# Optimization experiments

Measured on AMD Instinct MI355X. Metric: run time of the kernel, lower is better.

Reference implementation:

```python
import jax, jax.numpy as jnp
import numpy as np

B, S, H, NH = 2, 2048, 1024, 16
HD = H // NH  # head dim = 64


def setup_inputs() -> dict:
    key = jax.random.key(0)
    ks = jax.random.split(key, 11)
    s = 1.0 / np.sqrt(H)
    return {
        "q": jax.random.normal(ks[0], (B, S, H), jnp.float32),
        "k": jax.random.normal(ks[1], (B, S, H), jnp.float32),
        "v": jax.random.normal(ks[2], (B, S, H), jnp.float32),
        "Wq": jax.random.normal(ks[3], (H, H), jnp.float32) * s,
        "bq": jax.random.normal(ks[4], (H,), jnp.float32) * 0.02,
        "Wk": jax.random.normal(ks[5], (H, H), jnp.float32) * s,
        "bk": jax.random.normal(ks[6], (H,), jnp.float32) * 0.02,
        "Wv": jax.random.normal(ks[7], (H, H), jnp.float32) * s,
        "bv": jax.random.normal(ks[8], (H,), jnp.float32) * 0.02,
        "Wo": jax.random.normal(ks[9], (H, H), jnp.float32) * s,
        "bo": jax.random.normal(ks[10], (H,), jnp.float32) * 0.02,
    }


def reference(q, k, v, Wq, bq, Wk, bk, Wv, bv, Wo, bo):
    # QKV projections: [B,S,H]
    qp = q @ Wq + bq
    kp = k @ Wk + bk
    vp = v @ Wv + bv
    # split heads -> [B, NH, S, HD]
    def split(x):
        return x.reshape(B, S, NH, HD).transpose(0, 2, 1, 3)
    qh, kh, vh = split(qp), split(kp), split(vp)
    # scores [B, NH, S, S], scale by sqrt(head_dim)
    scores = jnp.einsum('bhqd,bhkd->bhqk', qh, kh) / jnp.sqrt(jnp.asarray(HD, qh.dtype))
    attn = jax.nn.softmax(scores, axis=-1)  # attention_dropout p=0.0 (eval)
    ctx = jnp.einsum('bhqk,bhkd->bhqd', attn, vh)
    # merge heads -> [B, S, H]
    ctx = ctx.transpose(0, 2, 1, 3).reshape(B, S, H)
    out = ctx @ Wo + bo  # dropout p=0.0 (eval)
    return out
```

## Files before the change

kernel.cpp:

```cpp
#include <hip/hip_runtime.h>

typedef unsigned short u16;
typedef __attribute__((ext_vector_type(8))) short bf16x8;
typedef __attribute__((ext_vector_type(4))) float f32x4;
typedef __attribute__((ext_vector_type(16))) float f32x16;
typedef __attribute__((ext_vector_type(4))) unsigned short u16x4;
typedef __attribute__((ext_vector_type(4))) unsigned int u32x4;

#define B_  2
#define S_  2048
#define H_  1024
#define NH_ 16
#define HD_ 64
#define MR_ (B_*S_)
#define K_  H_

__device__ __forceinline__ u16 f2bf(float f) {
  union { float f; unsigned u; } x; x.f = f;
  unsigned r = x.u + 0x7fffu + ((x.u >> 16) & 1u);
  return (u16)(r >> 16);
}

__device__ __forceinline__ unsigned cvtpk(float lo, float hi) {
  unsigned r;
  asm("v_cvt_pk_bf16_f32 %0, %1, %2" : "=v"(r) : "v"(lo), "v"(hi));
  return r;
}

__device__ __forceinline__ void plswap(unsigned &a, unsigned &b) {
  asm("v_permlane32_swap_b32 %0, %1" : "+v"(a), "+v"(b));
}

__device__ __forceinline__ void gload16(const u16* g, u16* l) {
  __builtin_amdgcn_global_load_lds((const __attribute__((address_space(1))) void*)g,
                                   (__attribute__((address_space(3))) void*)l, 16, 0, 0);
}

__global__ __launch_bounds__(256) void prep(const float* __restrict__ q, const float* __restrict__ k,
                                            const float* __restrict__ v, const float* __restrict__ Wq,
                                            const float* __restrict__ Wk, const float* __restrict__ Wv,
                                            const float* __restrict__ Wo, u16* __restrict__ dst,
                                            u16* __restrict__ wt) {
  __shared__ float t[32][33];
  const int bid = blockIdx.x;
  if (bid < 12288) {
    const int z = bid >> 12;
    const float* src = z == 0 ? q : z == 1 ? k : v;
    u16* d = dst + (size_t)z * MR_ * H_;
    size_t i = ((size_t)(bid & 4095) * 256 + threadIdx.x) * 4;
    float4 f = *(const float4*)(src + i);
    u16x4 o = { f2bf(f.x), f2bf(f.y), f2bf(f.z), f2bf(f.w) };
    *(u16x4*)(d + i) = o;
  } else {
    const int r = bid - 12288;
    const int z = r >> 10;
    const float* W = z == 0 ? Wq : z == 1 ? Wk : z == 2 ? Wv : Wo;
    u16* Wt = wt + (size_t)z * H_ * K_;
    const int n0 = (r & 31) * 32, k0 = ((r >> 5) & 31) * 32;
    const int tx = threadIdx.x & 31, ty = threadIdx.x >> 5;
    #pragma unroll
    for (int i = 0; i < 4; i++) t[ty + 8*i][tx] = W[(size_t)(k0 + ty + 8*i) * H_ + n0 + tx];
    __syncthreads();
    #pragma unroll
    for (int i = 0; i < 4; i++) Wt[(size_t)(n0 + ty + 8*i) * K_ + k0 + tx] = f2bf(t[tx][ty + 8*i]);
  }
}

template <int MODE>
__device__ __forceinline__ void gemm_body(const u16* __restrict__ A, const u16* __restrict__ Bt,
                                          const float* __restrict__ bias, float scale,
                                          u16* __restrict__ Obf, float* __restrict__ Of,
                                          int m_tile, int n_tile) {
  __shared__ u16 ldsA[128 * 64];
  __shared__ u16 ldsB[128 * 64];
  const int tid = threadIdx.x;
  const int lane = tid & 63, wave = tid >> 6;
  const int wm = wave >> 1, wn = wave & 1;
  const int m0 = m_tile * 128, n0 = n_tile * 128;

  f32x4 acc[4][4] = {};

  const int srow = tid >> 3;
  const int sslot = (tid & 7) ^ (srow & 7);
  const u16* ga = A + (size_t)(m0 + srow) * K_ + sslot * 8;
  const u16* gb = Bt + (size_t)(n0 + srow) * K_ + sslot * 8;
  u16* la = ldsA + tid * 8;
  u16* lb = ldsB + tid * 8;

  const int fr = lane & 15;
  const int kg = lane >> 4;

  for (int k0 = 0; k0 < K_; k0 += 64) {
    #pragma unroll
    for (int j = 0; j < 4; j++) gload16(ga + (size_t)(j * 32) * K_ + k0, la + j * 2048);
    #pragma unroll
    for (int j = 0; j < 4; j++) gload16(gb + (size_t)(j * 32) * K_ + k0, lb + j * 2048);
    __syncthreads();

    #pragma unroll
    for (int kk = 0; kk < 2; kk++) {
      const int ps = (((kk << 2) | kg) ^ (fr & 7)) * 8;
      bf16x8 a[4], b[4];
      #pragma unroll
      for (int mf = 0; mf < 4; mf++)
        a[mf] = *(const bf16x8*)&ldsA[(wm * 64 + mf * 16 + fr) * 64 + ps];
      #pragma unroll
      for (int nf = 0; nf < 4; nf++)
        b[nf] = *(const bf16x8*)&ldsB[(wn * 64 + nf * 16 + fr) * 64 + ps];
      #pragma unroll
      for (int mf = 0; mf < 4; mf++)
        #pragma unroll
        for (int nf = 0; nf < 4; nf++)
          acc[mf][nf] = __builtin_amdgcn_mfma_f32_16x16x32_bf16(a[mf], b[nf], acc[mf][nf], 0, 0, 0);
    }
    __syncthreads();
  }

  float bcol[4];
  #pragma unroll
  for (int nf = 0; nf < 4; nf++) bcol[nf] = bias[n0 + wn * 64 + nf * 16 + fr];

  if (MODE == 2) {
    #pragma unroll
    for (int mf = 0; mf < 4; mf++) {
      const int row0 = m0 + wm * 64 + mf * 16 + kg * 4;
      #pragma unroll
      for (int nf = 0; nf < 4; nf++) {
        const int col = n0 + wn * 64 + nf * 16 + fr;
        u16x4 o;
        #pragma unroll
        for (int r = 0; r < 4; r++) o[r] = f2bf(acc[mf][nf][r] + bcol[nf]);
        size_t idx = (((size_t)(col + ((row0 >> 11) << 10))) << 11) + (row0 & 2047);
        *(u16x4*)(Obf + idx) = o;
      }
    }
  } else {
    #pragma unroll
    for (int mf = 0; mf < 4; mf++)
      #pragma unroll
      for (int r = 0; r < 4; r++) {
        const int row = m0 + wm * 64 + mf * 16 + kg * 4 + r;
        #pragma unroll
        for (int nf = 0; nf < 4; nf++) {
          const int col = n0 + wn * 64 + nf * 16 + fr;
          float val = (acc[mf][nf][r] + bcol[nf]) * scale;
          if (MODE == 0) Obf[(size_t)row * H_ + col] = f2bf(val);
          else           Of [(size_t)row * H_ + col] = val;
        }
      }
  }
}

__device__ __forceinline__ void gemm_tiles(int &m_tile, int &n_tile) {
  const int bid = blockIdx.x + (blockIdx.y << 3);
  const int swz = ((bid & 7) << 5) + (bid >> 3);
  m_tile = swz >> 3;
  n_tile = swz & 7;
}

__global__ __launch_bounds__(256) void gemm_qkv(const u16* __restrict__ xb, const u16* __restrict__ wt,
                                                const float* __restrict__ b0, const float* __restrict__ b1,
                                                const float* __restrict__ b2,
                                                u16* __restrict__ QKo, u16* __restrict__ VTo) {
  const int z = blockIdx.z;
  const u16* A = xb + (size_t)z * MR_ * K_;
  const u16* Bt = wt + (size_t)z * H_ * K_;
  int mt, nt;
  gemm_tiles(mt, nt);
  if (z == 2) {
    gemm_body<2>(A, Bt, b2, 1.0f, VTo, nullptr, mt, nt);
  } else {
    const float* bias = z == 0 ? b0 : b1;
    const float scale = z == 0 ? 0.18033688011112042f : 1.0f;
    gemm_body<0>(A, Bt, bias, scale, QKo + (size_t)z * MR_ * H_, nullptr, mt, nt);
  }
}

__global__ __launch_bounds__(256) void gemm_out(const u16* __restrict__ ctx, const u16* __restrict__ wot,
                                                const float* __restrict__ bo, float* __restrict__ out) {
  int mt, nt;
  gemm_tiles(mt, nt);
  gemm_body<1>(ctx, wot, bo, 1.0f, nullptr, out, mt, nt);
}

__global__ __launch_bounds__(512, 4) void attn(const u16* __restrict__ qp, const u16* __restrict__ kp,
                                               const u16* __restrict__ vt, u16* __restrict__ ctx) {
  __shared__ u16 Kl[2][2][64 * 64];
  __shared__ u16 Vl[2][2][64 * 64];
  __shared__ float mlbuf[2][4][32][2];
  const int bid = blockIdx.x + (blockIdx.y << 4);
  const int swz = ((bid & 7) << 6) + (bid >> 3);
  const int bh = swz >> 4;
  const int b = bh >> 4, h = bh & 15;
  const int q0 = (swz & 15) * 128;
  const int tid = threadIdx.x;
  const int g0 = tid >> 8;
  const int gt = tid & 255;
  const int w = (tid >> 6) & 3;
  const int l = tid & 63;
  const int ql = l & 31, hi = l >> 5;

  const u16* Q   = qp + (size_t)b * S_ * H_ + h * HD_;
  const u16* Kb  = kp + (size_t)b * S_ * H_ + h * HD_;
  const u16* Vtb = vt + (size_t)bh * HD_ * S_;
  u16* O = ctx + (size_t)b * S_ * H_ + h * HD_;

  const int srow = gt >> 3;
  const int sslot = (gt & 7) ^ (srow & 7);
  const int sbase = g0 << 10;

  const u16* Qrow = Q + (size_t)(q0 + w * 32 + ql) * H_;

  f32x16 oacc0 = {}, oacc1 = {};
  float m_run = -1e30f, l_run = 0.f;

  #pragma unroll
  for (int j = 0; j < 2; j++) {
    gload16(Kb + (size_t)(sbase + srow + 32 * j) * H_ + sslot * 8,
            &Kl[g0][0][0] + j * 2048 + gt * 8);
    gload16(Vtb + (size_t)(srow + 32 * j) * S_ + sbase + sslot * 8,
            &Vl[g0][0][0] + j * 2048 + gt * 8);
  }

  for (int it = 0; it < 16; ++it) {
    const int s0 = sbase + it * 64, cur = it & 1;
    __syncthreads();
    if (it + 1 < 16) {
      #pragma unroll
      for (int j = 0; j < 2; j++) {
        gload16(Kb + (size_t)(s0 + 64 + srow + 32 * j) * H_ + sslot * 8,
                &Kl[g0][cur ^ 1][0] + j * 2048 + gt * 8);
        gload16(Vtb + (size_t)(srow + 32 * j) * S_ + s0 + 64 + sslot * 8,
                &Vl[g0][cur ^ 1][0] + j * 2048 + gt * 8);
      }
    }
    f32x16 sc0 = {}, sc1 = {};
    __builtin_amdgcn_s_setprio(1);
    #pragma unroll
    for (int ds = 0; ds < 4; ds++) {
      const int sl = ((ds * 2 + hi) ^ (ql & 7)) << 3;
      bf16x8 qd = *(const bf16x8*)&Qrow[ds * 16 + hi * 8];
      bf16x8 k0 = *(const bf16x8*)&Kl[g0][cur][ql * 64 + sl];
      bf16x8 k1 = *(const bf16x8*)&Kl[g0][cur][(32 + ql) * 64 + sl];
      sc0 = __builtin_amdgcn_mfma_f32_32x32x16_bf16(k0, qd, sc0, 0, 0, 0);
      sc1 = __builtin_amdgcn_mfma_f32_32x32x16_bf16(k1, qd, sc1, 0, 0, 0);
    }
    __builtin_amdgcn_s_setprio(0);
    float t4[8];
    #pragma unroll
    for (int g = 0; g < 4; g++) {
      t4[g]     = fmaxf(fmaxf(sc0[4*g], sc0[4*g+1]), fmaxf(sc0[4*g+2], sc0[4*g+3]));
      t4[4 + g] = fmaxf(fmaxf(sc1[4*g], sc1[4*g+1]), fmaxf(sc1[4*g+2], sc1[4*g+3]));
    }
    float tmax = fmaxf(fmaxf(fmaxf(t4[0], t4[1]), fmaxf(t4[2], t4[3])),
                       fmaxf(fmaxf(t4[4], t4[5]), fmaxf(t4[6], t4[7])));
    tmax = fmaxf(tmax, __shfl_xor(tmax, 32, 64));
    if (!__all(tmax <= m_run + 8.0f)) {
      const float mn = fmaxf(m_run, tmax);
      const float sf = __builtin_amdgcn_exp2f(m_run - mn);
      m_run = mn;
      l_run *= sf;
      #pragma unroll
      for (int r = 0; r < 16; r++) {
        const float sfq = __shfl(sf, (r & 3) + 8 * (r >> 2) + 4 * hi, 64);
        oacc0[r] *= sfq;
        oacc1[r] *= sfq;
      }
    }
    float ps4[8];
    #pragma unroll
    for (int g = 0; g < 4; g++) {
      #pragma unroll
      for (int m = 0; m < 4; m++) {
        sc0[4*g+m] = __builtin_amdgcn_exp2f(sc0[4*g+m] - m_run);
        sc1[4*g+m] = __builtin_amdgcn_exp2f(sc1[4*g+m] - m_run);
      }
      ps4[g]     = (sc0[4*g] + sc0[4*g+1]) + (sc0[4*g+2] + sc0[4*g+3]);
      ps4[4 + g] = (sc1[4*g] + sc1[4*g+1]) + (sc1[4*g+2] + sc1[4*g+3]);
    }
    float psum = ((ps4[0] + ps4[1]) + (ps4[2] + ps4[3])) + ((ps4[4] + ps4[5]) + (ps4[6] + ps4[7]));
    psum += __shfl_xor(psum, 32, 64);
    l_run += psum;
    uint2 pk0[4], pk1[4];
    #pragma unroll
    for (int g = 0; g < 4; g++) {
      pk0[g].x = cvtpk(sc0[4*g], sc0[4*g+1]);  pk0[g].y = cvtpk(sc0[4*g+2], sc0[4*g+3]);
      pk1[g].x = cvtpk(sc1[4*g], sc1[4*g+1]);  pk1[g].y = cvtpk(sc1[4*g+2], sc1[4*g+3]);
    }
    __builtin_amdgcn_s_setprio(1);
    #pragma unroll
    for (int ks = 0; ks < 4; ks++) {
      const int ga = (ks & 1) * 2;
      unsigned x0, y0, x1, y1;
      if (ks < 2) { x0 = pk0[ga].x; y0 = pk0[ga].y; x1 = pk0[ga+1].x; y1 = pk0[ga+1].y; }
      else        { x0 = pk1[ga].x; y0 = pk1[ga].y; x1 = pk1[ga+1].x; y1 = pk1[ga+1].y; }
      plswap(x0, x1);
      plswap(y0, y1);
      u32x4 fu = { x0, y0, x1, y1 };
      const bf16x8 pfrag = __builtin_bit_cast(bf16x8, fu);
      #pragma unroll
      for (int dt = 0; dt < 2; dt++) {
        const int d = dt * 32 + ql;
        bf16x8 vf = *(const bf16x8*)&Vl[g0][cur][d * 64 + (((ks * 2 + hi) ^ (d & 7)) << 3)];
        if (dt == 0) oacc0 = __builtin_amdgcn_mfma_f32_32x32x16_bf16(pfrag, vf, oacc0, 0, 0, 0);
        else         oacc1 = __builtin_amdgcn_mfma_f32_32x32x16_bf16(pfrag, vf, oacc1, 0, 0, 0);
      }
    }
    __builtin_amdgcn_s_setprio(0);
  }

  if (l < 32) { mlbuf[g0][w][ql][0] = m_run; mlbuf[g0][w][ql][1] = l_run; }
  __syncthreads();
  const float m_o = mlbuf[g0 ^ 1][w][ql][0];
  const float l_o = mlbuf[g0 ^ 1][w][ql][1];
  const float m_tot = fmaxf(m_run, m_o);
  const float a_s = __builtin_amdgcn_exp2f(m_run - m_tot);
  const float rinv = 1.0f / (l_run * a_s + l_o * __builtin_amdgcn_exp2f(m_o - m_tot));
  float ar[16], rr[16];
  #pragma unroll
  for (int r = 0; r < 16; r++) {
    const int qi = (r & 3) + 8 * (r >> 2) + 4 * hi;
    ar[r] = __shfl(a_s, qi, 64);
    rr[r] = __shfl(rinv, qi, 64);
  }

  float* cb = (float*)(&Kl[0][0][0]);
  float* cw = cb + w * 2048 + l;
  if (g0 == 1) {
    #pragma unroll
    for (int r = 0; r < 16; r++) {
      cw[r * 64]        = oacc0[r] * ar[r];
      cw[(16 + r) * 64] = oacc1[r] * ar[r];
    }
  }
  __syncthreads();
  if (g0 == 0) {
    #pragma unroll
    for (int r = 0; r < 16; r++) {
      const int qi = (r & 3) + 8 * (r >> 2) + 4 * hi;
      const int row = q0 + w * 32 + qi;
      O[(size_t)row * H_ + ql]      = f2bf((oacc0[r] * ar[r] + cw[r * 64]) * rr[r]);
      O[(size_t)row * H_ + 32 + ql] = f2bf((oacc1[r] * ar[r] + cw[(16 + r) * 64]) * rr[r]);
    }
  }
}

extern "C" void kernel_launch(void* const* d_in, const int* in_sizes, int n_in,
                              void* d_out, int out_size, void* d_ws, size_t ws_size,
                              hipStream_t stream) {
  const float* q  = (const float*)d_in[0];
  const float* k  = (const float*)d_in[1];
  const float* v  = (const float*)d_in[2];
  const float* Wq = (const float*)d_in[3];
  const float* bq = (const float*)d_in[4];
  const float* Wk = (const float*)d_in[5];
  const float* bk = (const float*)d_in[6];
  const float* Wv = (const float*)d_in[7];
  const float* bv = (const float*)d_in[8];
  const float* Wo = (const float*)d_in[9];
  const float* bo = (const float*)d_in[10];
  float* out = (float*)d_out;

  char* ws = (char*)d_ws;
  const size_t MB = 1024 * 1024;
  u16* xb   = (u16*)(ws);
  u16* wt   = (u16*)(ws + 24 * MB);
  u16* qkp  = (u16*)(ws + 32 * MB);
  u16* vtp  = (u16*)(ws + 48 * MB);
  u16* ctx  = (u16*)(ws);

  prep  <<<dim3(16384),      256, 0, stream>>>(q, k, v, Wq, Wk, Wv, Wo, xb, wt);
  gemm_qkv<<<dim3(8, 32, 3), 256, 0, stream>>>(xb, wt, bq, bk, bv, qkp, vtp);
  attn  <<<dim3(16, 32),     512, 0, stream>>>(qkp, qkp + (size_t)MR_ * H_, vtp, ctx);
  gemm_out<<<dim3(8, 32, 1), 256, 0, stream>>>(ctx, wt + (size_t)3 * H_ * K_, bo, out);
}
```

Baseline: 132.9 us.

## Use 256x256 double-buffered LDS tiles for the QKV projection GEMM

Replaces the 128x128 QKV GEMM with a 512-thread kernel computing 256x256 output tiles. It double-buffers A/B in LDS, issuing next-K-step global loads interleaved with MFMA phases and raising wave priority around the MFMAs. The larger tiles are meant to cut global/LDS traffic per FLOP and hide load latency. The cost is only 192 blocks, which may underfill the CUs, plus heavier register pressure and about 128KB of LDS per block. The output GEMM is split into its own f32-only body.

```diff
diff --git a/kernel.cpp b/kernel.cpp
--- a/kernel.cpp
+++ b/kernel.cpp
@@ -67,10 +67,143 @@
 }
 
 template <int MODE>
-__device__ __forceinline__ void gemm_body(const u16* __restrict__ A, const u16* __restrict__ Bt,
-                                          const float* __restrict__ bias, float scale,
-                                          u16* __restrict__ Obf, float* __restrict__ Of,
-                                          int m_tile, int n_tile) {
+__device__ __forceinline__ void body256(const u16* __restrict__ A, const u16* __restrict__ Bt,
+                                        const float* __restrict__ bias, float scale,
+                                        u16* __restrict__ Obf, int mt, int nt,
+                                        u16* lAbase, u16* lBbase) {
+  const int tid = threadIdx.x;
+  const int lane = tid & 63, wave = tid >> 6;
+  const int wm = wave >> 2, wn = wave & 3;
+  const int fr = lane & 15, kg = lane >> 4;
+  const int m0 = mt * 256, n0 = nt * 256;
+
+  const int srow = tid >> 3;
+  const int sslot = (tid & 7) ^ (srow & 7);
+  const u16* ga = A + (size_t)(m0 + srow) * K_ + sslot * 8;
+  const u16* gb = Bt + (size_t)(n0 + srow) * K_ + sslot * 8;
+
+  f32x4 acc[8][4] = {};
+
+  #pragma unroll
+  for (int j = 0; j < 4; j++) {
+    gload16(ga + (size_t)(j * 64) * K_, lAbase + j * 4096 + tid * 8);
+    gload16(gb + (size_t)(j * 64) * K_, lBbase + j * 4096 + tid * 8);
+  }
+  asm volatile("s_waitcnt vmcnt(0)" ::: "memory");
+  __builtin_amdgcn_s_barrier();
+  __builtin_amdgcn_sched_barrier(0);
+
+  for (int s = 0; s < 16; ++s) {
+    const int cur = s & 1;
+    const u16* Acur = lAbase + cur * 16384;
+    const u16* Bcur = lBbase + cur * 16384;
+    u16* Anxt = lAbase + (cur ^ 1) * 16384;
+    u16* Bnxt = lBbase + (cur ^ 1) * 16384;
+    const size_t knext = (size_t)(s + 1) * 64;
+    bf16x8 af[4][2];
+    #pragma unroll
+    for (int p = 0; p < 4; ++p) {
+      const int mh = p >> 1, nh = p & 1;
+      if ((p & 1) == 0) {
+        #pragma unroll
+        for (int mf2 = 0; mf2 < 4; ++mf2)
+          #pragma unroll
+          for (int kk = 0; kk < 2; ++kk)
+            af[mf2][kk] = *(const bf16x8*)&Acur[(wm * 128 + mh * 64 + mf2 * 16 + fr) * 64 +
+                                                ((((kk << 2) | kg) ^ (fr & 7)) << 3)];
+      }
+      bf16x8 bfr[2][2];
+      #pragma unroll
+      for (int nf2 = 0; nf2 < 2; ++nf2)
+        #pragma unroll
+        for (int kk = 0; kk < 2; ++kk)
+          bfr[nf2][kk] = *(const bf16x8*)&Bcur[(wn * 64 + nh * 32 + nf2 * 16 + fr) * 64 +
+                                               ((((kk << 2) | kg) ^ (fr & 7)) << 3)];
+      if (s < 15 && p < 2) {
+        #pragma unroll
+        for (int jj = 0; jj < 2; ++jj) {
+          const int j = p * 2 + jj;
+          gload16(ga + (size_t)(j * 64) * K_ + knext, Anxt + j * 4096 + tid * 8);
+          gload16(gb + (size_t)(j * 64) * K_ + knext, Bnxt + j * 4096 + tid * 8);
+        }
+      }
+      __builtin_amdgcn_s_barrier();
+      __builtin_amdgcn_s_setprio(1);
+      #pragma unroll
+      for (int mf2 = 0; mf2 < 4; ++mf2)
+        #pragma unroll
+        for (int nf2 = 0; nf2 < 2; ++nf2)
+          #pragma unroll
+          for (int kk = 0; kk < 2; ++kk)
+            acc[mh * 4 + mf2][nh * 2 + nf2] = __builtin_amdgcn_mfma_f32_16x16x32_bf16(
+                af[mf2][kk], bfr[nf2][kk], acc[mh * 4 + mf2][nh * 2 + nf2], 0, 0, 0);
+      __builtin_amdgcn_s_setprio(0);
+      if (p < 3) {
+        __builtin_amdgcn_s_barrier();
+      } else {
+        asm volatile("s_waitcnt vmcnt(0)" ::: "memory");
+        __builtin_amdgcn_s_barrier();
+        __builtin_amdgcn_sched_barrier(0);
+      }
+    }
+  }
+
+  float bcol[4];
+  #pragma unroll
+  for (int nf = 0; nf < 4; nf++) bcol[nf] = bias[n0 + wn * 64 + nf * 16 + fr];
+
+  if (MODE == 2) {
+    #pragma unroll
+    for (int mf = 0; mf < 8; mf++) {
+      const int row0 = m0 + wm * 128 + mf * 16 + kg * 4;
+      #pragma unroll
+      for (int nf = 0; nf < 4; nf++) {
+        const int col = n0 + wn * 64 + nf * 16 + fr;
+        u16x4 o;
+        #pragma unroll
+        for (int r = 0; r < 4; r++) o[r] = f2bf(acc[mf][nf][r] + bcol[nf]);
+        size_t idx = (((size_t)(col + ((row0 >> 11) << 10))) << 11) + (row0 & 2047);
+        *(u16x4*)(Obf + idx) = o;
+      }
+    }
+  } else {
+    #pragma unroll
+    for (int mf = 0; mf < 8; mf++)
+      #pragma unroll
+      for (int r = 0; r < 4; r++) {
+        const int row = m0 + wm * 128 + mf * 16 + kg * 4 + r;
+        #pragma unroll
+        for (int nf = 0; nf < 4; nf++) {
+          const int col = n0 + wn * 64 + nf * 16 + fr;
+          Obf[(size_t)row * H_ + col] = f2bf((acc[mf][nf][r] + bcol[nf]) * scale);
+        }
+      }
+  }
+}
+
+__global__ __launch_bounds__(512, 2) void gemm_qkv256(const u16* __restrict__ xb, const u16* __restrict__ wt,
+                                                      const float* __restrict__ b0, const float* __restrict__ b1,
+                                                      const float* __restrict__ b2,
+                                                      u16* __restrict__ QKo, u16* __restrict__ VTo) {
+  __shared__ u16 lA[2][256 * 64];
+  __shared__ u16 lB[2][256 * 64];
+  const int z = blockIdx.z;
+  const int swz = (blockIdx.x << 3) + blockIdx.y;
+  const int mt = swz >> 2, nt = swz & 3;
+  const u16* A = xb + (size_t)z * MR_ * K_;
+  const u16* Bt = wt + (size_t)z * H_ * K_;
+  if (z == 2) {
+    body256<2>(A, Bt, b2, 1.0f, VTo, mt, nt, &lA[0][0], &lB[0][0]);
+  } else {
+    const float* bias = z == 0 ? b0 : b1;
+    const float scale = z == 0 ? 0.18033688011112042f : 1.0f;
+    body256<0>(A, Bt, bias, scale, QKo + (size_t)z * MR_ * H_, mt, nt, &lA[0][0], &lB[0][0]);
+  }
+}
+
+__device__ __forceinline__ void gemm_body_f32(const u16* __restrict__ A, const u16* __restrict__ Bt,
+                                              const float* __restrict__ bias, float* __restrict__ Of,
+                                              int m_tile, int n_tile) {
   __shared__ u16 ldsA[128 * 64];
   __shared__ u16 ldsB[128 * 64];
   const int tid = threadIdx.x;
@@ -119,68 +252,24 @@
   float bcol[4];
   #pragma unroll
   for (int nf = 0; nf < 4; nf++) bcol[nf] = bias[n0 + wn * 64 + nf * 16 + fr];
-
-  if (MODE == 2) {
-    #pragma unroll
-    for (int mf = 0; mf < 4; mf++) {
-      const int row0 = m0 + wm * 64 + mf * 16 + kg * 4;
+  #pragma unroll
+  for (int mf = 0; mf < 4; mf++)
+    #pragma unroll
+    for (int r = 0; r < 4; r++) {
+      const int row = m0 + wm * 64 + mf * 16 + kg * 4 + r;
       #pragma unroll
       for (int nf = 0; nf < 4; nf++) {
         const int col = n0 + wn * 64 + nf * 16 + fr;
-        u16x4 o;
-        #pragma unroll
-        for (int r = 0; r < 4; r++) o[r] = f2bf(acc[mf][nf][r] + bcol[nf]);
-        size_t idx = (((size_t)(col + ((row0 >> 11) << 10))) << 11) + (row0 & 2047);
-        *(u16x4*)(Obf + idx) = o;
-      }
-    }
-  } else {
-    #pragma unroll
-    for (int mf = 0; mf < 4; mf++)
-      #pragma unroll
-      for (int r = 0; r < 4; r++) {
-        const int row = m0 + wm * 64 + mf * 16 + kg * 4 + r;
-        #pragma unroll
-        for (int nf = 0; nf < 4; nf++) {
-          const int col = n0 + wn * 64 + nf * 16 + fr;
-          float val = (acc[mf][nf][r] + bcol[nf]) * scale;
-          if (MODE == 0) Obf[(size_t)row * H_ + col] = f2bf(val);
-          else           Of [(size_t)row * H_ + col] = val;
-        }
-      }
-  }
-}
-
-__device__ __forceinline__ void gemm_tiles(int &m_tile, int &n_tile) {
+        Of[(size_t)row * H_ + col] = acc[mf][nf][r] + bcol[nf];
+      }
+    }
+}
+
+__global__ __launch_bounds__(256) void gemm_out(const u16* __restrict__ ctx, const u16* __restrict__ wot,
+                                                const float* __restrict__ bo, float* __restrict__ out) {
   const int bid = blockIdx.x + (blockIdx.y << 3);
   const int swz = ((bid & 7) << 5) + (bid >> 3);
-  m_tile = swz >> 3;
-  n_tile = swz & 7;
-}
-
-__global__ __launch_bounds__(256) void gemm_qkv(const u16* __restrict__ xb, const u16* __restrict__ wt,
-                                                const float* __restrict__ b0, const float* __restrict__ b1,
-                                                const float* __restrict__ b2,
-                                                u16* __restrict__ QKo, u16* __restrict__ VTo) {
-  const int z = blockIdx.z;
-  const u16* A = xb + (size_t)z * MR_ * K_;
-  const u16* Bt = wt + (size_t)z * H_ * K_;
-  int mt, nt;
-  gemm_tiles(mt, nt);
-  if (z == 2) {
-    gemm_body<2>(A, Bt, b2, 1.0f, VTo, nullptr, mt, nt);
-  } else {
-    const float* bias = z == 0 ? b0 : b1;
-    const float scale = z == 0 ? 0.18033688011112042f : 1.0f;
-    gemm_body<0>(A, Bt, bias, scale, QKo + (size_t)z * MR_ * H_, nullptr, mt, nt);
-  }
-}
-
-__global__ __launch_bounds__(256) void gemm_out(const u16* __restrict__ ctx, const u16* __restrict__ wot,
-                                                const float* __restrict__ bo, float* __restrict__ out) {
-  int mt, nt;
-  gemm_tiles(mt, nt);
-  gemm_body<1>(ctx, wot, bo, 1.0f, nullptr, out, mt, nt);
+  gemm_body_f32(ctx, wot, bo, out, swz >> 3, swz & 7);
 }
 
 __global__ __launch_bounds__(512, 4) void attn(const u16* __restrict__ qp, const u16* __restrict__ kp,
@@ -369,8 +458,8 @@
   u16* vtp  = (u16*)(ws + 48 * MB);
   u16* ctx  = (u16*)(ws);
 
-  prep  <<<dim3(16384),      256, 0, stream>>>(q, k, v, Wq, Wk, Wv, Wo, xb, wt);
-  gemm_qkv<<<dim3(8, 32, 3), 256, 0, stream>>>(xb, wt, bq, bk, bv, qkp, vtp);
-  attn  <<<dim3(16, 32),     512, 0, stream>>>(qkp, qkp + (size_t)MR_ * H_, vtp, ctx);
-  gemm_out<<<dim3(8, 32, 1), 256, 0, stream>>>(ctx, wt + (size_t)3 * H_ * K_, bo, out);
-}
+  prep      <<<dim3(16384),     256, 0, stream>>>(q, k, v, Wq, Wk, Wv, Wo, xb, wt);
+  gemm_qkv256<<<dim3(8, 8, 3),  512, 0, stream>>>(xb, wt, bq, bk, bv, qkp, vtp);
+  attn      <<<dim3(16, 32),    512, 0, stream>>>(qkp, qkp + (size_t)MR_ * H_, vtp, ctx);
+  gemm_out  <<<dim3(8, 32, 1),  256, 0, stream>>>(ctx, wt + (size_t)3 * H_ * K_, bo, out);
+}
```

After: 131.3 us (median of 2 runs). No clear change (-1.2%).

## Fuse fp32-to-bf16 activation conversion into QKV GEMM A-tile loads

Applied to the files above, without the earlier changes.

The prep kernel no longer converts q/k/v to bf16. The QKV GEMM instead reads fp32 activations into registers, packs them to bf16 with v_cvt_pk_bf16_f32, and writes them to LDS, prefetching the next k-slice while the MFMAs run. This removes the bf16 intermediate write and re-read of three 4096x1024 tensors. The cost is doubled A-tile global read bytes per GEMM tile, since each A tile is re-read by all 8 n-tiles in fp32, plus register-staged rather than direct-to-LDS loads.

```diff
diff --git a/kernel.cpp b/kernel.cpp
--- a/kernel.cpp
+++ b/kernel.cpp
@@ -36,43 +36,29 @@
                                    (__attribute__((address_space(3))) void*)l, 16, 0, 0);
 }
 
-__global__ __launch_bounds__(256) void prep(const float* __restrict__ q, const float* __restrict__ k,
-                                            const float* __restrict__ v, const float* __restrict__ Wq,
-                                            const float* __restrict__ Wk, const float* __restrict__ Wv,
-                                            const float* __restrict__ Wo, u16* __restrict__ dst,
+__global__ __launch_bounds__(256) void prep(const float* __restrict__ Wq, const float* __restrict__ Wk,
+                                            const float* __restrict__ Wv, const float* __restrict__ Wo,
                                             u16* __restrict__ wt) {
   __shared__ float t[32][33];
   const int bid = blockIdx.x;
-  if (bid < 12288) {
-    const int z = bid >> 12;
-    const float* src = z == 0 ? q : z == 1 ? k : v;
-    u16* d = dst + (size_t)z * MR_ * H_;
-    size_t i = ((size_t)(bid & 4095) * 256 + threadIdx.x) * 4;
-    float4 f = *(const float4*)(src + i);
-    u16x4 o = { f2bf(f.x), f2bf(f.y), f2bf(f.z), f2bf(f.w) };
-    *(u16x4*)(d + i) = o;
-  } else {
-    const int r = bid - 12288;
-    const int z = r >> 10;
-    const float* W = z == 0 ? Wq : z == 1 ? Wk : z == 2 ? Wv : Wo;
-    u16* Wt = wt + (size_t)z * H_ * K_;
-    const int n0 = (r & 31) * 32, k0 = ((r >> 5) & 31) * 32;
-    const int tx = threadIdx.x & 31, ty = threadIdx.x >> 5;
-    #pragma unroll
-    for (int i = 0; i < 4; i++) t[ty + 8*i][tx] = W[(size_t)(k0 + ty + 8*i) * H_ + n0 + tx];
-    __syncthreads();
-    #pragma unroll
-    for (int i = 0; i < 4; i++) Wt[(size_t)(n0 + ty + 8*i) * K_ + k0 + tx] = f2bf(t[tx][ty + 8*i]);
-  }
+  const int z = bid >> 10;
+  const int r = bid & 1023;
+  const float* W = z == 0 ? Wq : z == 1 ? Wk : z == 2 ? Wv : Wo;
+  u16* Wt = wt + (size_t)z * H_ * K_;
+  const int n0 = (r & 31) * 32, k0 = (r >> 5) * 32;
+  const int tx = threadIdx.x & 31, ty = threadIdx.x >> 5;
+  #pragma unroll
+  for (int i = 0; i < 4; i++) t[ty + 8*i][tx] = W[(size_t)(k0 + ty + 8*i) * H_ + n0 + tx];
+  __syncthreads();
+  #pragma unroll
+  for (int i = 0; i < 4; i++) Wt[(size_t)(n0 + ty + 8*i) * K_ + k0 + tx] = f2bf(t[tx][ty + 8*i]);
 }
 
 template <int MODE>
-__device__ __forceinline__ void gemm_body(const u16* __restrict__ A, const u16* __restrict__ Bt,
-                                          const float* __restrict__ bias, float scale,
-                                          u16* __restrict__ Obf, float* __restrict__ Of,
-                                          int m_tile, int n_tile) {
-  __shared__ u16 ldsA[128 * 64];
-  __shared__ u16 ldsB[128 * 64];
+__device__ __forceinline__ void qkv_body(const float* __restrict__ Af, const u16* __restrict__ Bt,
+                                         const float* __restrict__ bias, float scale,
+                                         u16* __restrict__ Obf, int m_tile, int n_tile,
+                                         u16* ldsA, u16* ldsB) {
   const int tid = threadIdx.x;
   const int lane = tid & 63, wave = tid >> 6;
   const int wm = wave >> 1, wn = wave & 1;
@@ -82,7 +68,7 @@
 
   const int srow = tid >> 3;
   const int sslot = (tid & 7) ^ (srow & 7);
-  const u16* ga = A + (size_t)(m0 + srow) * K_ + sslot * 8;
+  const float* gaf = Af + (size_t)(m0 + srow) * K_ + sslot * 8;
   const u16* gb = Bt + (size_t)(n0 + srow) * K_ + sslot * 8;
   u16* la = ldsA + tid * 8;
   u16* lb = ldsB + tid * 8;
@@ -90,12 +76,32 @@
   const int fr = lane & 15;
   const int kg = lane >> 4;
 
+  float4 alo[4], ahi[4];
+  #pragma unroll
+  for (int j = 0; j < 4; j++) {
+    const float* p = gaf + (size_t)(j * 32) * K_;
+    alo[j] = *(const float4*)p;
+    ahi[j] = *(const float4*)(p + 4);
+  }
+
   for (int k0 = 0; k0 < K_; k0 += 64) {
     #pragma unroll
-    for (int j = 0; j < 4; j++) gload16(ga + (size_t)(j * 32) * K_ + k0, la + j * 2048);
-    #pragma unroll
-    for (int j = 0; j < 4; j++) gload16(gb + (size_t)(j * 32) * K_ + k0, lb + j * 2048);
+    for (int j = 0; j < 4; j++) {
+      u32x4 wv = { cvtpk(alo[j].x, alo[j].y), cvtpk(alo[j].z, alo[j].w),
+                   cvtpk(ahi[j].x, ahi[j].y), cvtpk(ahi[j].z, ahi[j].w) };
+      *(u32x4*)(la + j * 2048) = wv;
+      gload16(gb + (size_t)(j * 32) * K_ + k0, lb + j * 2048);
+    }
     __syncthreads();
+
+    if (k0 + 64 < K_) {
+      #pragma unroll
+      for (int j = 0; j < 4; j++) {
+        const float* p = gaf + (size_t)(j * 32) * K_ + k0 + 64;
+        alo[j] = *(const float4*)p;
+        ahi[j] = *(const float4*)(p + 4);
+      }
+    }
 
     #pragma unroll
     for (int kk = 0; kk < 2; kk++) {
@@ -143,9 +149,7 @@
         #pragma unroll
         for (int nf = 0; nf < 4; nf++) {
           const int col = n0 + wn * 64 + nf * 16 + fr;
-          float val = (acc[mf][nf][r] + bcol[nf]) * scale;
-          if (MODE == 0) Obf[(size_t)row * H_ + col] = f2bf(val);
-          else           Of [(size_t)row * H_ + col] = val;
+          Obf[(size_t)row * H_ + col] = f2bf((acc[mf][nf][r] + bcol[nf]) * scale);
         }
       }
   }
@@ -158,29 +162,96 @@
   n_tile = swz & 7;
 }
 
-__global__ __launch_bounds__(256) void gemm_qkv(const u16* __restrict__ xb, const u16* __restrict__ wt,
+__global__ __launch_bounds__(256) void gemm_qkv(const float* __restrict__ q, const float* __restrict__ k,
+                                                const float* __restrict__ v, const u16* __restrict__ wt,
                                                 const float* __restrict__ b0, const float* __restrict__ b1,
                                                 const float* __restrict__ b2,
                                                 u16* __restrict__ QKo, u16* __restrict__ VTo) {
+  __shared__ u16 ldsA[128 * 64];
+  __shared__ u16 ldsB[128 * 64];
   const int z = blockIdx.z;
-  const u16* A = xb + (size_t)z * MR_ * K_;
-  const u16* Bt = wt + (size_t)z * H_ * K_;
   int mt, nt;
   gemm_tiles(mt, nt);
+  const float* A = z == 0 ? q : z == 1 ? k : v;
+  const u16* Bt = wt + (size_t)z * H_ * K_;
   if (z == 2) {
-    gemm_body<2>(A, Bt, b2, 1.0f, VTo, nullptr, mt, nt);
+    qkv_body<2>(A, Bt, b2, 1.0f, VTo, mt, nt, ldsA, ldsB);
   } else {
     const float* bias = z == 0 ? b0 : b1;
     const float scale = z == 0 ? 0.18033688011112042f : 1.0f;
-    gemm_body<0>(A, Bt, bias, scale, QKo + (size_t)z * MR_ * H_, nullptr, mt, nt);
-  }
+    qkv_body<0>(A, Bt, bias, scale, QKo + (size_t)z * MR_ * H_, mt, nt, ldsA, ldsB);
+  }
+}
+
+__device__ __forceinline__ void gemm_body_f32(const u16* __restrict__ A, const u16* __restrict__ Bt,
+                                              const float* __restrict__ bias, float* __restrict__ Of,
+                                              int m_tile, int n_tile) {
+  __shared__ u16 ldsA[128 * 64];
+  __shared__ u16 ldsB[128 * 64];
+  const int tid = threadIdx.x;
+  const int lane = tid & 63, wave = tid >> 6;
+  const int wm = wave >> 1, wn = wave & 1;
+  const int m0 = m_tile * 128, n0 = n_tile * 128;
+
+  f32x4 acc[4][4] = {};
+
+  const int srow = tid >> 3;
+  const int sslot = (tid & 7) ^ (srow & 7);
+  const u16* ga = A + (size_t)(m0 + srow) * K_ + sslot * 8;
+  const u16* gb = Bt + (size_t)(n0 + srow) * K_ + sslot * 8;
+  u16* la = ldsA + tid * 8;
+  u16* lb = ldsB + tid * 8;
+
+  const int fr = lane & 15;
+  const int kg = lane >> 4;
+
+  for (int k0 = 0; k0 < K_; k0 += 64) {
+    #pragma unroll
+    for (int j = 0; j < 4; j++) gload16(ga + (size_t)(j * 32) * K_ + k0, la + j * 2048);
+    #pragma unroll
+    for (int j = 0; j < 4; j++) gload16(gb + (size_t)(j * 32) * K_ + k0, lb + j * 2048);
+    __syncthreads();
+
+    #pragma unroll
+    for (int kk = 0; kk < 2; kk++) {
+      const int ps = (((kk << 2) | kg) ^ (fr & 7)) * 8;
+      bf16x8 a[4], b[4];
+      #pragma unroll
+      for (int mf = 0; mf < 4; mf++)
+        a[mf] = *(const bf16x8*)&ldsA[(wm * 64 + mf * 16 + fr) * 64 + ps];
+      #pragma unroll
+      for (int nf = 0; nf < 4; nf++)
+        b[nf] = *(const bf16x8*)&ldsB[(wn * 64 + nf * 16 + fr) * 64 + ps];
+      #pragma unroll
+      for (int mf = 0; mf < 4; mf++)
+        #pragma unroll
+        for (int nf = 0; nf < 4; nf++)
+          acc[mf][nf] = __builtin_amdgcn_mfma_f32_16x16x32_bf16(a[mf], b[nf], acc[mf][nf], 0, 0, 0);
+    }
+    __syncthreads();
+  }
+
+  float bcol[4];
+  #pragma unroll
+  for (int nf = 0; nf < 4; nf++) bcol[nf] = bias[n0 + wn * 64 + nf * 16 + fr];
+  #pragma unroll
+  for (int mf = 0; mf < 4; mf++)
+    #pragma unroll
+    for (int r = 0; r < 4; r++) {
+      const int row = m0 + wm * 64 + mf * 16 + kg * 4 + r;
+      #pragma unroll
+      for (int nf = 0; nf < 4; nf++) {
+        const int col = n0 + wn * 64 + nf * 16 + fr;
+        Of[(size_t)row * H_ + col] = acc[mf][nf][r] + bcol[nf];
+      }
+    }
 }
 
 __global__ __launch_bounds__(256) void gemm_out(const u16* __restrict__ ctx, const u16* __restrict__ wot,
                                                 const float* __restrict__ bo, float* __restrict__ out) {
-  int mt, nt;
-  gemm_tiles(mt, nt);
-  gemm_body<1>(ctx, wot, bo, 1.0f, nullptr, out, mt, nt);
+  const int bid = blockIdx.x + (blockIdx.y << 3);
+  const int swz = ((bid & 7) << 5) + (bid >> 3);
+  gemm_body_f32(ctx, wot, bo, out, swz >> 3, swz & 7);
 }
 
 __global__ __launch_bounds__(512, 4) void attn(const u16* __restrict__ qp, const u16* __restrict__ kp,
@@ -363,14 +434,13 @@
 
   char* ws = (char*)d_ws;
   const size_t MB = 1024 * 1024;
-  u16* xb   = (u16*)(ws);
+  u16* ctx  = (u16*)(ws);
   u16* wt   = (u16*)(ws + 24 * MB);
   u16* qkp  = (u16*)(ws + 32 * MB);
   u16* vtp  = (u16*)(ws + 48 * MB);
-  u16* ctx  = (u16*)(ws);
-
-  prep  <<<dim3(16384),      256, 0, stream>>>(q, k, v, Wq, Wk, Wv, Wo, xb, wt);
-  gemm_qkv<<<dim3(8, 32, 3), 256, 0, stream>>>(xb, wt, bq, bk, bv, qkp, vtp);
-  attn  <<<dim3(16, 32),     512, 0, stream>>>(qkp, qkp + (size_t)MR_ * H_, vtp, ctx);
-  gemm_out<<<dim3(8, 32, 1), 256, 0, stream>>>(ctx, wt + (size_t)3 * H_ * K_, bo, out);
-}
+
+  prep    <<<dim3(4096),      256, 0, stream>>>(Wq, Wk, Wv, Wo, wt);
+  gemm_qkv<<<dim3(8, 32, 3),  256, 0, stream>>>(q, k, v, wt, bq, bk, bv, qkp, vtp);
+  attn    <<<dim3(16, 32),    512, 0, stream>>>(qkp, qkp + (size_t)MR_ * H_, vtp, ctx);
+  gemm_out<<<dim3(8, 32, 1),  256, 0, stream>>>(ctx, wt + (size_t)3 * H_ * K_, bo, out);
+}
```

After: 133.8 us. About the same (+0.7%).
